# Optimization experiments

Measured on AMD Instinct MI355X. Metric: run time of the kernel, lower is better.

## Reference

```python
import jax, jax.numpy as jnp
import numpy as np

E = 8   # num routed experts
K = 1   # top-k per token
D = 512   # embed_dim
I = 2048  # moe_inter_dim (= 4*D)
B, T = 2, 2048


def setup_inputs() -> dict:
    key = jax.random.key(0)
    ks = jax.random.split(key, 7)
    s = 0.02
    x = jax.random.normal(ks[0], (B, T, D), jnp.float32)
    gate_w = jax.random.normal(ks[1], (E, D), jnp.float32) * s      # TopKGate.proj.weight
    w1 = jax.random.normal(ks[2], (E, I, D), jnp.float32) * s       # Expert.w1.weight per expert
    w2 = jax.random.normal(ks[3], (E, D, I), jnp.float32) * s       # Expert.w2.weight
    w3 = jax.random.normal(ks[4], (E, I, D), jnp.float32) * s       # Expert.w3.weight
    sw1 = jax.random.normal(ks[5], (I, D), jnp.float32) * s         # shared Linear(dim -> 1*inter)
    sw2 = jax.random.normal(ks[6], (D, I), jnp.float32) * s         # shared Linear(inter -> dim)
    return {"x": x, "gate_w": gate_w, "w1": w1, "w2": w2, "w3": w3, "sw1": sw1, "sw2": sw2}


def reference(x, gate_w, w1, w2, w3, sw1, sw2):
    xf = x.reshape(-1, D)                                  # [N, D]
    # gate: logits -> topk -> softmax over selected logits
    logits = xf @ gate_w.T                                 # [N, E]
    wts, idx = jax.lax.top_k(logits, K)                    # [N, K]
    wts = jax.nn.softmax(wts, axis=-1)
    # per-token combine weight for each expert (0 if not routed) -- identical
    # math to the torch gather/scatter loop, fully vectorized over experts.
    comb = jnp.einsum('nke,nk->ne', jax.nn.one_hot(idx, E, dtype=xf.dtype), wts)  # [N, E]
    # SwiGLU experts, batched over the expert axis
    h = jax.nn.silu(jnp.einsum('nd,eid->nei', xf, w1)) * jnp.einsum('nd,eid->nei', xf, w3)  # [N, E, I]
    y = jnp.einsum('nei,edi->nd', h * comb[:, :, None], w2)  # weighted combine
    # shared expert: Linear -> GELU(exact) -> Linear
    y = y + jax.nn.gelu(xf @ sw1.T, approximate=False) @ sw2.T
    return y.reshape(x.shape)
```

## Files before the change

### kernel.cpp

```cpp
#include <hip/hip_runtime.h>
#include <hip/hip_bf16.h>
#include <math.h>

#define N_TOK 4096
#define DIM 512
#define IDIM 2048
#define NEXP 8

#define W1_ELS 8388608
#define W3_ELS 8388608
#define W2_ELS 8388608
#define SW1_ELS 1048576
#define SW2_ELS 1048576
#define CONV_ELS 27262976
#define CONV_CHUNKS 3407872
#define GATE_BLOCKS 256
#define CONV_BLOCKS 2048
#define CONV_THREADS (CONV_BLOCKS * 256)

typedef __attribute__((ext_vector_type(8))) short bf16x8;
typedef __attribute__((ext_vector_type(4))) float floatx4;

__device__ __forceinline__ short f2bf(float f) {
  unsigned int u;
  __builtin_memcpy(&u, &f, 4);
  u += 0x7fff + ((u >> 16) & 1);
  return (short)(u >> 16);
}

__device__ __forceinline__ bf16x8 ld8f(const float* __restrict__ p) {
  float4 a = *(const float4*)p;
  float4 b = *(const float4*)(p + 4);
  bf16x8 v;
  v[0] = f2bf(a.x); v[1] = f2bf(a.y); v[2] = f2bf(a.z); v[3] = f2bf(a.w);
  v[4] = f2bf(b.x); v[5] = f2bf(b.y); v[6] = f2bf(b.z); v[7] = f2bf(b.w);
  return v;
}

__device__ __forceinline__ float gelu_exactish(float v) {
  float z = fabsf(v) * 0.70710678118f;
  float tt = 1.f / (1.f + 0.3275911f * z);
  float poly = tt * (0.254829592f + tt * (-0.284496736f + tt * (1.421413741f +
               tt * (-1.453152027f + tt * 1.061405429f))));
  float er = 1.f - poly * __expf(-z * z);
  er = (v < 0.f) ? -er : er;
  return 0.5f * v * (1.f + er);
}

__device__ __forceinline__ void gll(const short* g, short* l) {
  __builtin_amdgcn_global_load_lds(
      (const __attribute__((address_space(1))) void*)g,
      (__attribute__((address_space(3))) void*)l, 16, 0, 0);
}

__global__ __launch_bounds__(256) void gate_conv_kernel(
    const float* __restrict__ x, const float* __restrict__ gw,
    short* __restrict__ xb, int* __restrict__ expert_id,
    const float* __restrict__ w1, const float* __restrict__ w3,
    const float* __restrict__ w2, const float* __restrict__ sw1,
    const float* __restrict__ sw2,
    short* __restrict__ w1b, short* __restrict__ w3b, short* __restrict__ w2b,
    short* __restrict__ sw1b, short* __restrict__ sw2b) {
  __shared__ float xs[16 * 516];
  __shared__ double ps[16][8][2];
  int t = threadIdx.x;

  if (blockIdx.x >= GATE_BLOCKS) {
    long tidg = (long)(blockIdx.x - GATE_BLOCKS) * 256 + t;
    for (long c = tidg; c < CONV_CHUNKS; c += CONV_THREADS) {
      long i = c * 8;
      const float* src;
      short* dst;
      long off;
      if (i < W1_ELS)                          { src = w1;  dst = w1b;  off = i; }
      else if (i < 2L * W1_ELS)                { src = w3;  dst = w3b;  off = i - W1_ELS; }
      else if (i < 3L * W1_ELS)                { src = w2;  dst = w2b;  off = i - 2L * W1_ELS; }
      else if (i < 3L * W1_ELS + SW1_ELS)      { src = sw1; dst = sw1b; off = i - 3L * W1_ELS; }
      else                                     { src = sw2; dst = sw2b; off = i - 3L * W1_ELS - SW1_ELS; }
      *(bf16x8*)(dst + off) = ld8f(src + off);
    }
    return;
  }

  int tok0 = blockIdx.x * 16;
  const float* xrow = x + (long)tok0 * DIM;
  for (int i = t; i < 2048; i += 256) {
    float4 v = ((const float4*)xrow)[i];
    int row = i >> 7, c4 = i & 127;
    *(float4*)&xs[row * 516 + c4 * 4] = v;
    short4 b;
    b.x = f2bf(v.x); b.y = f2bf(v.y); b.z = f2bf(v.z); b.w = f2bf(v.w);
    *(short4*)(xb + (long)tok0 * DIM + i * 4) = b;
  }
  __syncthreads();
  int tok = t & 15, e = (t >> 4) & 7, hf = t >> 7;
  const float* xr = &xs[tok * 516 + hf * 256];
  const float* wr = gw + e * DIM + hf * 256;
  double s = 0.0;
  for (int k = 0; k < 256; k += 4) {
    float4 xv = *(const float4*)(xr + k);
    float4 wv = *(const float4*)(wr + k);
    s += (double)xv.x * wv.x + (double)xv.y * wv.y +
         (double)xv.z * wv.z + (double)xv.w * wv.w;
  }
  ps[tok][e][hf] = s;
  __syncthreads();
  if (t < 16) {
    double best = ps[t][0][0] + ps[t][0][1];
    int bi = 0;
#pragma unroll
    for (int j = 1; j < 8; j++) {
      double v = ps[t][j][0] + ps[t][j][1];
      if (v > best) { best = v; bi = j; }
    }
    expert_id[tok0 + t] = bi;
  }
}

__global__ __launch_bounds__(256) void scan_scatter(
    const int* __restrict__ expert_id, int* __restrict__ counts,
    int* __restrict__ offsets, int* __restrict__ cursors, int* __restrict__ nmeta,
    int* __restrict__ te1, int* __restrict__ tr1,
    int* __restrict__ te2, int* __restrict__ tr2, int* __restrict__ perm) {
  __shared__ int cnt[8];
  __shared__ int scur[8];
  int tid = threadIdx.x;
  if (tid < 8) cnt[tid] = 0;
  __syncthreads();
  int eid[16];
#pragma unroll
  for (int j = 0; j < 16; j++) {
    eid[j] = expert_id[tid + j * 256];
    atomicAdd(&cnt[eid[j]], 1);
  }
  __syncthreads();
  if (tid == 0) {
    int acc = 0;
    for (int e = 0; e < NEXP; e++) {
      counts[e] = cnt[e];
      offsets[e] = acc;
      scur[e] = acc;
      acc += cnt[e];
    }
    int n1 = 0;
    for (int e = 0; e < NEXP; e++)
      for (int r = 0; r < cnt[e]; r += 128) { te1[n1] = e; tr1[n1] = r; n1++; }
    for (int r = 0; r < N_TOK; r += 128) { te1[n1] = 8; tr1[n1] = r; n1++; }
    int n2 = 0;
    for (int e = 0; e < NEXP; e++)
      for (int r = 0; r < cnt[e]; r += 64) { te2[n2] = e; tr2[n2] = r; n2++; }
    nmeta[0] = n1;
    nmeta[1] = n2;
  }
  __syncthreads();
#pragma unroll
  for (int j = 0; j < 16; j++) {
    int slot = atomicAdd(&scur[eid[j]], 1);
    perm[slot] = tid + j * 256;
  }
}

__global__ __launch_bounds__(256, 4) void stage1(
    const short* __restrict__ xb, const short* __restrict__ w1b,
    const short* __restrict__ w3b, const short* __restrict__ sw1b,
    short* __restrict__ h, short* __restrict__ g,
    const int* __restrict__ counts, const int* __restrict__ offsets,
    const int* __restrict__ nmeta, const int* __restrict__ te,
    const int* __restrict__ tr, const int* __restrict__ perm) {
  __shared__ short Al[128 * 64];
  __shared__ short B1l[64 * 64];
  __shared__ short B2l[64 * 64];
  int t = blockIdx.y;
  if (t >= nmeta[0]) return;
  int e = te[t], row0 = tr[t];
  bool routed = (e < 8);
  int cnt = routed ? counts[e] : N_TOK;
  int base = routed ? offsets[e] : 0;
  int n0 = blockIdx.x * 64;
  int tid = threadIdx.x, lane = tid & 63, w = tid >> 6;
  int wm = w >> 1, wn = w & 1;
  const short* B1 = routed ? w1b + (long)e * IDIM * DIM : sw1b;
  const short* B2 = w3b + (long)e * IDIM * DIM;

  int aoff[4], lbA[4];
#pragma unroll
  for (int j = 0; j < 4; j++) {
    int c = w * 256 + j * 64 + lane;
    int row = c >> 3, klog = (c & 7) ^ (row & 7);
    int srow = row0 + row;
    int slot = base + ((srow < cnt) ? srow : (cnt - 1));
    aoff[j] = perm[slot] * DIM + klog * 8;
    lbA[j] = (w * 256 + j * 64) * 8;
  }
  int bgoff[2], lbB[2];
#pragma unroll
  for (int i = 0; i < 2; i++) {
    int c = i * 256 + tid;
    int row = c >> 3, klog = (c & 7) ^ (row & 7);
    bgoff[i] = (n0 + row) * DIM + klog * 8;
    lbB[i] = (i * 256 + w * 64) * 8;
  }

  floatx4 acc[2][4][2];
#pragma unroll
  for (int m = 0; m < 2; m++)
#pragma unroll
    for (int i = 0; i < 4; i++)
#pragma unroll
      for (int j = 0; j < 2; j++) acc[m][i][j] = (floatx4)0.f;

  for (int kc = 0; kc < DIM; kc += 64) {
#pragma unroll
    for (int j = 0; j < 4; j++) gll(xb + aoff[j] + kc, &Al[lbA[j]]);
#pragma unroll
    for (int i = 0; i < 2; i++) gll(B1 + bgoff[i] + kc, &B1l[lbB[i]]);
    if (routed) {
#pragma unroll
      for (int i = 0; i < 2; i++) gll(B2 + bgoff[i] + kc, &B2l[lbB[i]]);
    }
    __syncthreads();

#pragma unroll
    for (int kf = 0; kf < 2; kf++) {
      int kp = (kf * 4 + (lane >> 4)) ^ (lane & 7);
      bf16x8 af[4];
#pragma unroll
      for (int mf = 0; mf < 4; mf++) {
        int row = wm * 64 + mf * 16 + (lane & 15);
        af[mf] = *(const bf16x8*)&Al[row * 64 + kp * 8];
      }
#pragma unroll
      for (int nf = 0; nf < 2; nf++) {
        int col = wn * 32 + nf * 16 + (lane & 15);
        bf16x8 b1 = *(const bf16x8*)&B1l[col * 64 + kp * 8];
#pragma unroll
        for (int mf = 0; mf < 4; mf++)
          acc[0][mf][nf] = __builtin_amdgcn_mfma_f32_16x16x32_bf16(
              af[mf], b1, acc[0][mf][nf], 0, 0, 0);
        if (routed) {
          bf16x8 b2 = *(const bf16x8*)&B2l[col * 64 + kp * 8];
#pragma unroll
          for (int mf = 0; mf < 4; mf++)
            acc[1][mf][nf] = __builtin_amdgcn_mfma_f32_16x16x32_bf16(
                af[mf], b2, acc[1][mf][nf], 0, 0, 0);
        }
      }
    }
    __syncthreads();
  }

  short* S = Al;
  int quad = lane >> 4;
  short* dst = routed ? h : g;
#pragma unroll
  for (int mf = 0; mf < 4; mf++)
#pragma unroll
    for (int r = 0; r < 4; r++) {
      int lr = wm * 64 + mf * 16 + quad * 4 + r;
      int sw = ((lr >> 2) & 3) << 4;
#pragma unroll
      for (int nf = 0; nf < 2; nf++) {
        int lc = wn * 32 + nf * 16 + (lane & 15);
        float a1 = acc[0][mf][nf][r];
        short v;
        if (routed) {
          float a3 = acc[1][mf][nf][r];
          v = f2bf((a1 / (1.f + __expf(-a1))) * a3);
        } else {
          v = f2bf(gelu_exactish(a1));
        }
        S[lr * 64 + ((lc & 48) ^ sw) + (lc & 15)] = v;
      }
    }
  __syncthreads();
#pragma unroll
  for (int pass = 0; pass < 2; pass++) {
    int lr = pass * 64 + (tid >> 2);
    int srow = row0 + lr;
    if (srow < cnt) {
      int p = (tid & 3) * 16;
      int lcs = p ^ (((lr >> 2) & 3) << 4);
      bf16x8 v0 = *(const bf16x8*)&S[lr * 64 + lcs];
      bf16x8 v1 = *(const bf16x8*)&S[lr * 64 + lcs + 8];
      long ro = (long)(base + srow) * IDIM + n0 + p;
      *(bf16x8*)&dst[ro] = v0;
      *(bf16x8*)&dst[ro + 8] = v1;
    }
  }
}

__global__ __launch_bounds__(256, 8) void stage2(
    const short* __restrict__ h, const short* __restrict__ g,
    const short* __restrict__ w2b, const short* __restrict__ sw2b,
    float* __restrict__ out, const int* __restrict__ counts,
    const int* __restrict__ offsets, const int* __restrict__ nmeta,
    const int* __restrict__ te, const int* __restrict__ tr,
    const int* __restrict__ perm) {
  __shared__ short Al[64 * 64];
  __shared__ short Bl[32 * 64];
  int lid = blockIdx.x + 16 * blockIdx.y;
  int logical = (lid & 7) * 144 + (lid >> 3);
  int t = logical >> 4;
  int n0 = (logical & 15) * 32;
  if (t >= nmeta[1]) return;
  int e = te[t], row0 = tr[t];
  int cnt = counts[e], base = offsets[e];
  const short* w2e = w2b + (long)e * DIM * IDIM;
  int tid = threadIdx.x, lane = tid & 63, w = tid >> 6;
  int wm = w >> 1, wn = w & 1;

  int aoff[2], lbA[2];
#pragma unroll
  for (int i = 0; i < 2; i++) {
    int c = i * 256 + tid;
    int row = c >> 3, klog = (c & 7) ^ (row & 7);
    int srow = row0 + row;
    int arow = base + ((srow < cnt) ? srow : (cnt - 1));
    aoff[i] = arow * IDIM + klog * 8;
    lbA[i] = (i * 256 + w * 64) * 8;
  }
  int brow = tid >> 3, bklog = (tid & 7) ^ (brow & 7);
  int bgoff = (n0 + brow) * IDIM + bklog * 8;
  int lbB = (w * 64) * 8;

  floatx4 acc[2];
  acc[0] = (floatx4)0.f;
  acc[1] = (floatx4)0.f;

#pragma unroll
  for (int ph = 0; ph < 2; ph++) {
    const short* As = ph ? g : h;
    const short* Bs = ph ? sw2b : w2e;
    for (int kc = 0; kc < IDIM; kc += 64) {
#pragma unroll
      for (int i = 0; i < 2; i++) gll(As + aoff[i] + kc, &Al[lbA[i]]);
      gll(Bs + bgoff + kc, &Bl[lbB]);
      __syncthreads();

#pragma unroll
      for (int kf = 0; kf < 2; kf++) {
        int kp = (kf * 4 + (lane >> 4)) ^ (lane & 7);
        int col = wn * 16 + (lane & 15);
        bf16x8 bv = *(const bf16x8*)&Bl[col * 64 + kp * 8];
#pragma unroll
        for (int mf = 0; mf < 2; mf++) {
          int row = wm * 32 + mf * 16 + (lane & 15);
          bf16x8 af = *(const bf16x8*)&Al[row * 64 + kp * 8];
          acc[mf] = __builtin_amdgcn_mfma_f32_16x16x32_bf16(
              af, bv, acc[mf], 0, 0, 0);
        }
      }
      __syncthreads();
    }
  }

  int quad = lane >> 4;
  int colb = n0 + wn * 16 + (lane & 15);
#pragma unroll
  for (int mf = 0; mf < 2; mf++)
#pragma unroll
    for (int r = 0; r < 4; r++) {
      int srow = row0 + wm * 32 + mf * 16 + quad * 4 + r;
      if (srow >= cnt) continue;
      long ro = (long)perm[base + srow] * DIM + colb;
      out[ro] = acc[mf][r];
    }
}

extern "C" void kernel_launch(void* const* d_in, const int* in_sizes, int n_in,
                              void* d_out, int out_size, void* d_ws, size_t ws_size,
                              hipStream_t stream) {
  const float* x = (const float*)d_in[0];
  const float* gate_w = (const float*)d_in[1];
  const float* w1 = (const float*)d_in[2];
  const float* w2 = (const float*)d_in[3];
  const float* w3 = (const float*)d_in[4];
  const float* sw1 = (const float*)d_in[5];
  const float* sw2 = (const float*)d_in[6];
  float* out = (float*)d_out;

  char* ws = (char*)d_ws;
  int* counts = (int*)ws;
  int* offsets = counts + 8;
  int* cursors = offsets + 8;
  int* nmeta = cursors + 8;
  int* te1 = nmeta + 8;
  int* tr1 = te1 + 128;
  int* te2 = tr1 + 128;
  int* tr2 = te2 + 128;
  int* expert_id = tr2 + 128;
  int* perm = expert_id + N_TOK;
  short* xb = (short*)(ws + 65536);
  short* h = xb + (size_t)N_TOK * DIM;
  short* g = h + (size_t)N_TOK * IDIM;
  short* w1b = g + (size_t)N_TOK * IDIM;
  short* w3b = w1b + (size_t)W1_ELS;
  short* w2b = w3b + (size_t)W3_ELS;
  short* sw1b = w2b + (size_t)W2_ELS;
  short* sw2b = sw1b + (size_t)SW1_ELS;

  gate_conv_kernel<<<GATE_BLOCKS + CONV_BLOCKS, 256, 0, stream>>>(
      x, gate_w, xb, expert_id, w1, w3, w2, sw1, sw2,
      w1b, w3b, w2b, sw1b, sw2b);
  scan_scatter<<<1, 256, 0, stream>>>(expert_id, counts, offsets, cursors, nmeta,
                                      te1, tr1, te2, tr2, perm);
  stage1<<<dim3(IDIM / 64, 72), 256, 0, stream>>>(
      xb, w1b, w3b, sw1b, h, g, counts, offsets, nmeta, te1, tr1, perm);
  stage2<<<dim3(16, 72), 256, 0, stream>>>(
      h, g, w2b, sw2b, out, counts, offsets, nmeta, te2, tr2, perm);
}
```

Baseline: 243.2 us.

## Double-buffer B tiles and register-prefetch A tiles in stage1 GEMM

Stage1's K loop now prefetches the next chunk while the current one runs on MFMAs. The weight tiles go through ping-pong LDS buffers via direct global-to-LDS loads, and the activation tile is staged through registers and written to LDS after a barrier. The goal is to hide global memory latency behind compute. In exchange it uses more LDS and registers, so occupancy drops from 4 to 3 blocks per CU and a second barrier is added per iteration.

```diff
diff --git a/kernel.cpp b/kernel.cpp
--- a/kernel.cpp
+++ b/kernel.cpp
@@ -160,7 +160,7 @@
   }
 }
 
-__global__ __launch_bounds__(256, 4) void stage1(
+__global__ __launch_bounds__(256, 3) void stage1(
     const short* __restrict__ xb, const short* __restrict__ w1b,
     const short* __restrict__ w3b, const short* __restrict__ sw1b,
     short* __restrict__ h, short* __restrict__ g,
@@ -168,8 +168,8 @@
     const int* __restrict__ nmeta, const int* __restrict__ te,
     const int* __restrict__ tr, const int* __restrict__ perm) {
   __shared__ short Al[128 * 64];
-  __shared__ short B1l[64 * 64];
-  __shared__ short B2l[64 * 64];
+  __shared__ short B1l[2][64 * 64];
+  __shared__ short B2l[2][64 * 64];
   int t = blockIdx.y;
   if (t >= nmeta[0]) return;
   int e = te[t], row0 = tr[t];
@@ -209,16 +209,37 @@
 #pragma unroll
       for (int j = 0; j < 2; j++) acc[m][i][j] = (floatx4)0.f;
 
+  int4 areg[4];
+#pragma unroll
+  for (int j = 0; j < 4; j++)
+    areg[j] = *(const int4*)(xb + aoff[j]);
+#pragma unroll
+  for (int i = 0; i < 2; i++) gll(B1 + bgoff[i], &B1l[0][lbB[i]]);
+  if (routed) {
+#pragma unroll
+    for (int i = 0; i < 2; i++) gll(B2 + bgoff[i], &B2l[0][lbB[i]]);
+  }
+#pragma unroll
+  for (int j = 0; j < 4; j++)
+    *(int4*)&Al[lbA[j] + lane * 8] = areg[j];
+  __syncthreads();
+
   for (int kc = 0; kc < DIM; kc += 64) {
-#pragma unroll
-    for (int j = 0; j < 4; j++) gll(xb + aoff[j] + kc, &Al[lbA[j]]);
-#pragma unroll
-    for (int i = 0; i < 2; i++) gll(B1 + bgoff[i] + kc, &B1l[lbB[i]]);
-    if (routed) {
-#pragma unroll
-      for (int i = 0; i < 2; i++) gll(B2 + bgoff[i] + kc, &B2l[lbB[i]]);
-    }
-    __syncthreads();
+    int b = (kc >> 6) & 1;
+    bool pf = (kc + 64 < DIM);
+    if (pf) {
+#pragma unroll
+      for (int j = 0; j < 4; j++)
+        areg[j] = *(const int4*)(xb + aoff[j] + kc + 64);
+#pragma unroll
+      for (int i = 0; i < 2; i++)
+        gll(B1 + bgoff[i] + kc + 64, &B1l[b ^ 1][lbB[i]]);
+      if (routed) {
+#pragma unroll
+        for (int i = 0; i < 2; i++)
+          gll(B2 + bgoff[i] + kc + 64, &B2l[b ^ 1][lbB[i]]);
+      }
+    }
 
 #pragma unroll
     for (int kf = 0; kf < 2; kf++) {
@@ -232,19 +253,25 @@
 #pragma unroll
       for (int nf = 0; nf < 2; nf++) {
         int col = wn * 32 + nf * 16 + (lane & 15);
-        bf16x8 b1 = *(const bf16x8*)&B1l[col * 64 + kp * 8];
+        bf16x8 b1 = *(const bf16x8*)&B1l[b][col * 64 + kp * 8];
 #pragma unroll
         for (int mf = 0; mf < 4; mf++)
           acc[0][mf][nf] = __builtin_amdgcn_mfma_f32_16x16x32_bf16(
               af[mf], b1, acc[0][mf][nf], 0, 0, 0);
         if (routed) {
-          bf16x8 b2 = *(const bf16x8*)&B2l[col * 64 + kp * 8];
+          bf16x8 b2 = *(const bf16x8*)&B2l[b][col * 64 + kp * 8];
 #pragma unroll
           for (int mf = 0; mf < 4; mf++)
             acc[1][mf][nf] = __builtin_amdgcn_mfma_f32_16x16x32_bf16(
                 af[mf], b2, acc[1][mf][nf], 0, 0, 0);
         }
       }
+    }
+    __syncthreads();
+    if (pf) {
+#pragma unroll
+      for (int j = 0; j < 4; j++)
+        *(int4*)&Al[lbA[j] + lane * 8] = areg[j];
     }
     __syncthreads();
   }
```

Measured after the change: 291.7 us. 20.0% more time.

## Double-buffer stage1 LDS tiles and shrink M tile to 64 rows

Applied to the files above, without the earlier changes.

Stage1 now uses ping-pong LDS buffers for the A, W1 and W3 tiles, so global-to-LDS loads for the next K chunk are issued while MFMAs run on the current one. This removes one barrier per iteration and hides load latency. The row tile shrinks from 128 to 64 tokens, which doubles the tile count (grid y grows to 136, metadata arrays to 256) and gives better load balance across uneven expert counts. The cost is less weight reuse per block, more total B-tile traffic, and lower occupancy from the launch bound of 3.

```diff
diff --git a/kernel.cpp b/kernel.cpp
--- a/kernel.cpp
+++ b/kernel.cpp
@@ -144,8 +144,8 @@
     }
     int n1 = 0;
     for (int e = 0; e < NEXP; e++)
-      for (int r = 0; r < cnt[e]; r += 128) { te1[n1] = e; tr1[n1] = r; n1++; }
-    for (int r = 0; r < N_TOK; r += 128) { te1[n1] = 8; tr1[n1] = r; n1++; }
+      for (int r = 0; r < cnt[e]; r += 64) { te1[n1] = e; tr1[n1] = r; n1++; }
+    for (int r = 0; r < N_TOK; r += 64) { te1[n1] = 8; tr1[n1] = r; n1++; }
     int n2 = 0;
     for (int e = 0; e < NEXP; e++)
       for (int r = 0; r < cnt[e]; r += 64) { te2[n2] = e; tr2[n2] = r; n2++; }
@@ -160,16 +160,19 @@
   }
 }
 
-__global__ __launch_bounds__(256, 4) void stage1(
+__global__ __launch_bounds__(256, 3) void stage1(
     const short* __restrict__ xb, const short* __restrict__ w1b,
     const short* __restrict__ w3b, const short* __restrict__ sw1b,
     short* __restrict__ h, short* __restrict__ g,
     const int* __restrict__ counts, const int* __restrict__ offsets,
     const int* __restrict__ nmeta, const int* __restrict__ te,
     const int* __restrict__ tr, const int* __restrict__ perm) {
-  __shared__ short Al[128 * 64];
-  __shared__ short B1l[64 * 64];
-  __shared__ short B2l[64 * 64];
+  __shared__ short Al0[64 * 64];
+  __shared__ short Al1[64 * 64];
+  __shared__ short B1l0[64 * 64];
+  __shared__ short B1l1[64 * 64];
+  __shared__ short B2l0[64 * 64];
+  __shared__ short B2l1[64 * 64];
   int t = blockIdx.y;
   if (t >= nmeta[0]) return;
   int e = te[t], row0 = tr[t];
@@ -182,65 +185,78 @@
   const short* B1 = routed ? w1b + (long)e * IDIM * DIM : sw1b;
   const short* B2 = w3b + (long)e * IDIM * DIM;
 
-  int aoff[4], lbA[4];
-#pragma unroll
-  for (int j = 0; j < 4; j++) {
-    int c = w * 256 + j * 64 + lane;
+  int aoff[2], bgoff[2], lb[2];
+#pragma unroll
+  for (int i = 0; i < 2; i++) {
+    int c = i * 256 + tid;
     int row = c >> 3, klog = (c & 7) ^ (row & 7);
     int srow = row0 + row;
     int slot = base + ((srow < cnt) ? srow : (cnt - 1));
-    aoff[j] = perm[slot] * DIM + klog * 8;
-    lbA[j] = (w * 256 + j * 64) * 8;
-  }
-  int bgoff[2], lbB[2];
-#pragma unroll
-  for (int i = 0; i < 2; i++) {
-    int c = i * 256 + tid;
-    int row = c >> 3, klog = (c & 7) ^ (row & 7);
+    aoff[i] = perm[slot] * DIM + klog * 8;
     bgoff[i] = (n0 + row) * DIM + klog * 8;
-    lbB[i] = (i * 256 + w * 64) * 8;
-  }
-
-  floatx4 acc[2][4][2];
+    lb[i] = (i * 256 + w * 64) * 8;
+  }
+
+  floatx4 acc[2][2][2];
 #pragma unroll
   for (int m = 0; m < 2; m++)
 #pragma unroll
-    for (int i = 0; i < 4; i++)
+    for (int i = 0; i < 2; i++)
 #pragma unroll
       for (int j = 0; j < 2; j++) acc[m][i][j] = (floatx4)0.f;
 
-  for (int kc = 0; kc < DIM; kc += 64) {
-#pragma unroll
-    for (int j = 0; j < 4; j++) gll(xb + aoff[j] + kc, &Al[lbA[j]]);
-#pragma unroll
-    for (int i = 0; i < 2; i++) gll(B1 + bgoff[i] + kc, &B1l[lbB[i]]);
-    if (routed) {
-#pragma unroll
-      for (int i = 0; i < 2; i++) gll(B2 + bgoff[i] + kc, &B2l[lbB[i]]);
-    }
-    __syncthreads();
+#pragma unroll
+  for (int i = 0; i < 2; i++) gll(xb + aoff[i], &Al0[lb[i]]);
+#pragma unroll
+  for (int i = 0; i < 2; i++) gll(B1 + bgoff[i], &B1l0[lb[i]]);
+  if (routed) {
+#pragma unroll
+    for (int i = 0; i < 2; i++) gll(B2 + bgoff[i], &B2l0[lb[i]]);
+  }
+  __syncthreads();
+
+#pragma unroll
+  for (int ki = 0; ki < 8; ki++) {
+    const int kc = ki * 64;
+    short* An = (ki & 1) ? Al0 : Al1;
+    short* B1n = (ki & 1) ? B1l0 : B1l1;
+    short* B2n = (ki & 1) ? B2l0 : B2l1;
+    const short* Ac = (ki & 1) ? Al1 : Al0;
+    const short* B1c = (ki & 1) ? B1l1 : B1l0;
+    const short* B2c = (ki & 1) ? B2l1 : B2l0;
+
+    if (ki < 7) {
+#pragma unroll
+      for (int i = 0; i < 2; i++) gll(xb + aoff[i] + kc + 64, &An[lb[i]]);
+#pragma unroll
+      for (int i = 0; i < 2; i++) gll(B1 + bgoff[i] + kc + 64, &B1n[lb[i]]);
+      if (routed) {
+#pragma unroll
+        for (int i = 0; i < 2; i++) gll(B2 + bgoff[i] + kc + 64, &B2n[lb[i]]);
+      }
+    }
 
 #pragma unroll
     for (int kf = 0; kf < 2; kf++) {
       int kp = (kf * 4 + (lane >> 4)) ^ (lane & 7);
-      bf16x8 af[4];
-#pragma unroll
-      for (int mf = 0; mf < 4; mf++) {
-        int row = wm * 64 + mf * 16 + (lane & 15);
-        af[mf] = *(const bf16x8*)&Al[row * 64 + kp * 8];
+      bf16x8 af[2];
+#pragma unroll
+      for (int mf = 0; mf < 2; mf++) {
+        int row = wm * 32 + mf * 16 + (lane & 15);
+        af[mf] = *(const bf16x8*)&Ac[row * 64 + kp * 8];
       }
 #pragma unroll
       for (int nf = 0; nf < 2; nf++) {
         int col = wn * 32 + nf * 16 + (lane & 15);
-        bf16x8 b1 = *(const bf16x8*)&B1l[col * 64 + kp * 8];
-#pragma unroll
-        for (int mf = 0; mf < 4; mf++)
+        bf16x8 b1 = *(const bf16x8*)&B1c[col * 64 + kp * 8];
+#pragma unroll
+        for (int mf = 0; mf < 2; mf++)
           acc[0][mf][nf] = __builtin_amdgcn_mfma_f32_16x16x32_bf16(
               af[mf], b1, acc[0][mf][nf], 0, 0, 0);
         if (routed) {
-          bf16x8 b2 = *(const bf16x8*)&B2l[col * 64 + kp * 8];
-#pragma unroll
-          for (int mf = 0; mf < 4; mf++)
+          bf16x8 b2 = *(const bf16x8*)&B2c[col * 64 + kp * 8];
+#pragma unroll
+          for (int mf = 0; mf < 2; mf++)
             acc[1][mf][nf] = __builtin_amdgcn_mfma_f32_16x16x32_bf16(
                 af[mf], b2, acc[1][mf][nf], 0, 0, 0);
         }
@@ -249,14 +265,14 @@
     __syncthreads();
   }
 
-  short* S = Al;
+  short* S = Al0;
   int quad = lane >> 4;
   short* dst = routed ? h : g;
 #pragma unroll
-  for (int mf = 0; mf < 4; mf++)
+  for (int mf = 0; mf < 2; mf++)
 #pragma unroll
     for (int r = 0; r < 4; r++) {
-      int lr = wm * 64 + mf * 16 + quad * 4 + r;
+      int lr = wm * 32 + mf * 16 + quad * 4 + r;
       int sw = ((lr >> 2) & 3) << 4;
 #pragma unroll
       for (int nf = 0; nf < 2; nf++) {
@@ -273,9 +289,8 @@
       }
     }
   __syncthreads();
-#pragma unroll
-  for (int pass = 0; pass < 2; pass++) {
-    int lr = pass * 64 + (tid >> 2);
+  {
+    int lr = tid >> 2;
     int srow = row0 + lr;
     if (srow < cnt) {
       int p = (tid & 3) * 16;
@@ -385,10 +400,10 @@
   int* cursors = offsets + 8;
   int* nmeta = cursors + 8;
   int* te1 = nmeta + 8;
-  int* tr1 = te1 + 128;
-  int* te2 = tr1 + 128;
-  int* tr2 = te2 + 128;
-  int* expert_id = tr2 + 128;
+  int* tr1 = te1 + 256;
+  int* te2 = tr1 + 256;
+  int* tr2 = te2 + 256;
+  int* expert_id = tr2 + 256;
   int* perm = expert_id + N_TOK;
   short* xb = (short*)(ws + 65536);
   short* h = xb + (size_t)N_TOK * DIM;
@@ -404,7 +419,7 @@
       w1b, w3b, w2b, sw1b, sw2b);
   scan_scatter<<<1, 256, 0, stream>>>(expert_id, counts, offsets, cursors, nmeta,
                                       te1, tr1, te2, tr2, perm);
-  stage1<<<dim3(IDIM / 64, 72), 256, 0, stream>>>(
+  stage1<<<dim3(IDIM / 64, 136), 256, 0, stream>>>(
       xb, w1b, w3b, sw1b, h, g, counts, offsets, nmeta, te1, tr1, perm);
   stage2<<<dim3(16, 72), 256, 0, stream>>>(
       h, g, w2b, sw2b, out, counts, offsets, nmeta, te2, tr2, perm);
```

Result: no change. 242.4 us (-0.3%).
